# Performance work log

Hardware: AMD Instinct MI355X
Metric: run time of the kernel (lower is better)

## Reference

```python
import jax, jax.numpy as jnp
import numpy as np

B, S, D, H, DK, F, L, FEAT, T = 32, 256, 512, 8, 64, 2048, 6, 9, 100


def _pos_emb(seq_len, d):
    # 'transformers from scratch' style sinusoidal embedding
    pos = jnp.arange(seq_len, dtype=jnp.float32)[:, None]
    dim = jnp.arange(d, dtype=jnp.float32)[None, :]
    phase = pos / jnp.power(1e4, dim / d)
    return jnp.where(jnp.arange(d)[None, :] % 2 == 0, jnp.sin(phase), jnp.cos(phase))


def _ln(x, g, b, eps=1e-5):
    m = jnp.mean(x, -1, keepdims=True)
    v = jnp.mean((x - m) ** 2, -1, keepdims=True)
    return (x - m) * jax.lax.rsqrt(v + eps) * g + b


def _mha(q_in, k_in, v_in, wq, bq, wk, bk, wv, bv, wo, bo):
    # wq/wk/wv: [H, D, DK]; batched equivalent of per-head Linear projections
    q = jnp.einsum('bsd,hdk->bhsk', q_in, wq) + bq[:, None, :]
    k = jnp.einsum('bsd,hdk->bhsk', k_in, wk) + bk[:, None, :]
    v = jnp.einsum('bsd,hdk->bhsk', v_in, wv) + bv[:, None, :]
    scale = jnp.sqrt(jnp.asarray(q.shape[-1], jnp.float32))
    att = jax.nn.softmax(jnp.einsum('bhqk,bhsk->bhqs', q, k) / scale, axis=-1)
    o = jnp.einsum('bhqs,bhsv->bhqv', att, v)  # [B,H,S,DK]
    o = o.transpose(0, 2, 1, 3).reshape(q_in.shape[0], q_in.shape[1], -1)  # concat heads
    return o @ wo + bo


def setup_inputs() -> dict:
    key = jax.random.key(0)
    ks = iter(jax.random.split(key, 64))
    rn = lambda *sh: 0.02 * jax.random.normal(next(ks), sh, jnp.float32)
    d = {
        'tgt': jax.random.uniform(next(ks), (B, S, FEAT), jnp.float32),
        'memory': jax.random.normal(next(ks), (B, S, D), jnp.float32),
        'time': jax.random.randint(next(ks), (B, S), 0, T),
        'gender': jax.random.randint(next(ks), (B, 1), 0, 2),
        'race': jax.random.randint(next(ks), (B, 1), 0, 3),
        'mask': jax.random.uniform(next(ks), (B, S, FEAT), jnp.float32),
        'w_f2h': rn(FEAT, D), 'b_f2h': jnp.zeros((D,)),
        'emb_time': rn(T, D), 'emb_gender': rn(2, D), 'emb_race': rn(3, D),
        'wq1': rn(L, H, D, DK), 'bq1': jnp.zeros((L, H, DK)),
        'wk1': rn(L, H, D, DK), 'bk1': jnp.zeros((L, H, DK)),
        'wv1': rn(L, H, D, DK), 'bv1': jnp.zeros((L, H, DK)),
        'wo1': rn(L, H * DK, D), 'bo1': jnp.zeros((L, D)),
        'g1': jnp.ones((L, D)), 'be1': jnp.zeros((L, D)),
        'wq2': rn(L, H, D, DK), 'bq2': jnp.zeros((L, H, DK)),
        'wk2': rn(L, H, D, DK), 'bk2': jnp.zeros((L, H, DK)),
        'wv2': rn(L, H, D, DK), 'bv2': jnp.zeros((L, H, DK)),
        'wo2': rn(L, H * DK, D), 'bo2': jnp.zeros((L, D)),
        'g2': jnp.ones((L, D)), 'be2': jnp.zeros((L, D)),
        'w1f': rn(L, D, F), 'b1f': jnp.zeros((L, F)),
        'w2f': rn(L, F, D), 'b2f': jnp.zeros((L, D)),
        'gf': jnp.ones((L, D)), 'bff': jnp.zeros((L, D)),
        'w_out': rn(D, FEAT), 'b_out': jnp.zeros((FEAT,)),
        'w_m': rn(D, FEAT), 'b_m': jnp.zeros((FEAT,)),
    }
    return d


def reference(tgt, memory, time, gender, race, mask,
              w_f2h, b_f2h, emb_time, emb_gender, emb_race,
              wq1, bq1, wk1, bk1, wv1, bv1, wo1, bo1, g1, be1,
              wq2, bq2, wk2, bk2, wv2, bv2, wo2, bo2, g2, be2,
              w1f, b1f, w2f, b2f, gf, bff,
              w_out, b_out, w_m, b_m):
    # attentioned_mask=False, mask provided -> tgt = tgt * mask
    x = (tgt * mask) @ w_f2h + b_f2h  # feature2hidden
    x = x + _pos_emb(x.shape[1], x.shape[2])
    x = x + emb_time[time] + emb_gender[gender] + emb_race[race]  # [B,S,D] += [B,1,D]
    for l in range(L):
        # self-attention residual block (dropout is identity in eval)
        x = _ln(x + _mha(x, x, x, wq1[l], bq1[l], wk1[l], bk1[l], wv1[l], bv1[l], wo1[l], bo1[l]), g1[l], be1[l])
        # 'cross' block: q,k from memory, v from tgt; residual on tgt (tensors[-1])
        x = _ln(x + _mha(memory, memory, x, wq2[l], bq2[l], wk2[l], bk2[l], wv2[l], bv2[l], wo2[l], bo2[l]), g2[l], be2[l])
        # feed forward
        x = _ln(x + jax.nn.relu(x @ w1f[l] + b1f[l]) @ w2f[l] + b2f[l], gf[l], bff[l])
    output = jax.nn.sigmoid(x @ w_out + b_out)
    mask_out = jax.nn.sigmoid(x @ w_m + b_m)  # attentioned_mask=False -> linear_m(tgt)
    return output, time, mask_out
```

## Files before the change

### kernel.cpp

```cpp
#include <hip/hip_runtime.h>
#include <hip/hip_bf16.h>
#include <math.h>

constexpr int Bn   = 32;
constexpr int Sn   = 256;
constexpr int Dn   = 512;
constexpr int Hn   = 8;
constexpr int DKn  = 64;
constexpr int Fn   = 2048;
constexpr int Ln   = 6;
constexpr int FEATn= 9;
constexpr int BSn  = Bn * Sn;

typedef __hip_bfloat16 bf16;
typedef __attribute__((ext_vector_type(8))) short short8;
typedef __attribute__((ext_vector_type(4))) short short4v;
typedef __attribute__((ext_vector_type(4))) float f32x4;

#define GLOAD_LDS16(gp, lp)                                                   \
    __builtin_amdgcn_global_load_lds(                                         \
        (const __attribute__((address_space(1))) void*)(gp),                  \
        (__attribute__((address_space(3))) void*)(lp), 16, 0, 0)

#define BARRIER do {                                                          \
    __builtin_amdgcn_sched_barrier(0);                                        \
    asm volatile("" ::: "memory");                                            \
    __builtin_amdgcn_s_barrier();                                             \
    asm volatile("" ::: "memory");                                            \
    __builtin_amdgcn_sched_barrier(0);                                        \
} while (0)

#define VMCNT0 do {                                                           \
    asm volatile("s_waitcnt vmcnt(0)" ::: "memory");                          \
    __builtin_amdgcn_sched_barrier(0);                                        \
} while (0)

#define LGKM0 do {                                                            \
    asm volatile("s_waitcnt lgkmcnt(0)" ::: "memory");                        \
    __builtin_amdgcn_sched_barrier(0);                                        \
} while (0)

__device__ __forceinline__ short f2bs(float f) {
    __hip_bfloat16 h = __float2bfloat16(f);
    return *reinterpret_cast<short*>(&h);
}
__device__ __forceinline__ float bs2f(short s) {
    unsigned u = ((unsigned)(unsigned short)s) << 16;
    return *reinterpret_cast<float*>(&u);
}

__global__ __launch_bounds__(256)
void k_embed(const float* __restrict__ tgt, const float* __restrict__ mask,
             const float* __restrict__ w_f2h, const float* __restrict__ b_f2h,
             const int* __restrict__ timei, const int* __restrict__ gender,
             const int* __restrict__ race,
             const float* __restrict__ emb_t, const float* __restrict__ emb_g,
             const float* __restrict__ emb_r, bf16* __restrict__ x)
{
    int idx = blockIdx.x * 256 + threadIdx.x;
    int d  = idx & (Dn - 1);
    int bs = idx >> 9;
    int b  = bs / Sn;
    int s  = bs & (Sn - 1);
    const float* tg = tgt  + (size_t)bs * FEATn;
    const float* mk = mask + (size_t)bs * FEATn;
    float acc = b_f2h[d];
    #pragma unroll
    for (int f = 0; f < FEATn; ++f) acc += tg[f] * mk[f] * w_f2h[f * Dn + d];
    float phase = (float)s * expf(-((float)d / (float)Dn) * 9.210340372f);
    acc += (d & 1) ? cosf(phase) : sinf(phase);
    acc += emb_t[(size_t)timei[bs] * Dn + d];
    acc += emb_g[(size_t)gender[b] * Dn + d];
    acc += emb_r[(size_t)race[b]   * Dn + d];
    x[idx] = __float2bfloat16(acc);
}

__global__ __launch_bounds__(256)
void k_cvt(const float* __restrict__ in, bf16* __restrict__ out)
{
    int i = blockIdx.x * 256 + threadIdx.x;
    out[i] = __float2bfloat16(in[i]);
}

__global__ __launch_bounds__(256)
void k_tcvt6(const float* __restrict__ i0, bf16* __restrict__ o0,
             const float* __restrict__ i1, bf16* __restrict__ o1,
             const float* __restrict__ i2, bf16* __restrict__ o2,
             const float* __restrict__ i3, bf16* __restrict__ o3,
             const float* __restrict__ i4, bf16* __restrict__ o4,
             const float* __restrict__ i5, bf16* __restrict__ o5,
             int R, int C, int ZB)
{
    __shared__ float ts[32][33];
    const int sel = blockIdx.z / ZB, zi = blockIdx.z % ZB;
    const float* in  = sel == 0 ? i0 : sel == 1 ? i1 : sel == 2 ? i2
                     : sel == 3 ? i3 : sel == 4 ? i4 : i5;
    bf16*        out = sel == 0 ? o0 : sel == 1 ? o1 : sel == 2 ? o2
                     : sel == 3 ? o3 : sel == 4 ? o4 : o5;
    const int t  = threadIdx.x;
    const int tx = t & 31, ty = t >> 5;
    const int r0 = blockIdx.y * 32, c0 = blockIdx.x * 32;
    const size_t zo = (size_t)zi * R * C;
    #pragma unroll
    for (int i = 0; i < 4; ++i)
        ts[ty + 8 * i][tx] = in[zo + (size_t)(r0 + ty + 8 * i) * C + c0 + tx];
    __syncthreads();
    #pragma unroll
    for (int i = 0; i < 4; ++i)
        out[zo + (size_t)(c0 + ty + 8 * i) * R + r0 + tx] =
            __float2bfloat16(ts[tx][ty + 8 * i]);
}

__global__ __launch_bounds__(256)
void k_prep_final(const float* __restrict__ w_out, const float* __restrict__ b_out,
                  const float* __restrict__ w_m, const float* __restrict__ b_m,
                  bf16* __restrict__ Wcat, float* __restrict__ bcat)
{
    int idx = blockIdx.x * 256 + threadIdx.x;
    int n = idx >> 9, k = idx & 511;
    float v = 0.f;
    if (n < FEATn)          v = w_out[(size_t)k * FEATn + n];
    else if (n < 2 * FEATn) v = w_m[(size_t)k * FEATn + (n - FEATn)];
    Wcat[idx] = __float2bfloat16(v);
    if (idx < 32) {
        float bv = idx < FEATn ? b_out[idx]
                 : (idx < 2 * FEATn ? b_m[idx - FEATn] : 0.f);
        bcat[idx] = bv;
    }
}

template<int BN, bool RELU, bool RESID>
__global__ __launch_bounds__(256)
void k_gemm2ph(const bf16* __restrict__ Ain, const bf16* __restrict__ Win,
               const float* __restrict__ bia, const bf16* __restrict__ Rr,
               bf16* __restrict__ Cout, int M, int N, int K, int MTt, int NTt)
{
    constexpr int NT   = BN / 32;
    constexpr int NCB  = BN / 32;
    constexpr int BSZ  = BN * 64;
    constexpr int CSTR = BN + 8;
    constexpr int CPR  = BN / 8;
    __shared__ __align__(16) short smem[8192 + 2 * BSZ];

    const int id = blockIdx.x;
    const int cx = id & 7, j = id >> 3;
    const int mt = cx * (MTt >> 3) + j / NTt;
    const int nt = j % NTt;
    const int m0 = mt * 64, n0 = nt * BN;

    const int t = threadIdx.x, w = t >> 6, lane = t & 63;
    const int l16 = lane & 15, quad = lane >> 4;
    const int wm = (w & 1) * 32, wn = (w >> 1) * (BN / 2);

    const short* A = (const short*)Ain;
    const short* W = (const short*)Win;

    const int rowL = t >> 3;
    const int cX   = (t & 7) ^ (rowL & 7);
    const short* pA0 = A + (size_t)(m0 +  0 + rowL) * K + cX * 8;
    const short* pA1 = A + (size_t)(m0 + 32 + rowL) * K + cX * 8;
    const short* pB[NCB];
    #pragma unroll
    for (int i = 0; i < NCB; ++i)
        pB[i] = W + (size_t)(n0 + i * 32 + rowL) * K + cX * 8;

    auto stage = [&](int nb, int k2) {
        short* dA = smem + nb * 4096 + t * 8;
        short* dB = smem + 8192 + nb * BSZ + t * 8;
        GLOAD_LDS16(pA0 + (size_t)k2 * 64, dA);
        GLOAD_LDS16(pA1 + (size_t)k2 * 64, dA + 2048);
        #pragma unroll
        for (int i = 0; i < NCB; ++i)
            GLOAD_LDS16(pB[i] + (size_t)k2 * 64, dB + i * 2048);
    };

    const int axor  = (quad ^ (l16 & 7)) << 3;
    const int aBase = (wm + l16) * 64 + axor;
    const int bBase = 8192 + (wn + l16) * 64 + axor;

    float bias_v[NT];
    #pragma unroll
    for (int ni = 0; ni < NT; ++ni)
        bias_v[ni] = bia[n0 + wn + ni * 16 + l16];

    f32x4 acc[2][NT] = {};

    stage(0, 0);
    VMCNT0;
    BARRIER;

    const int NKT = K >> 6;
    for (int kt = 0; kt < NKT; ++kt) {
        const int bufA = (kt & 1) * 4096;
        const int bufB = (kt & 1) * BSZ;
        short8 af[2][2], bw[2][NT];
        #pragma unroll
        for (int mi = 0; mi < 2; ++mi) {
            const int a0 = bufA + aBase + mi * 1024;
            af[0][mi] = *(const short8*)(smem + a0);
            af[1][mi] = *(const short8*)(smem + (a0 ^ 32));
        }
        #pragma unroll
        for (int ni = 0; ni < NT; ++ni) {
            const int b0 = bufB + bBase + ni * 1024;
            bw[0][ni] = *(const short8*)(smem + b0);
            bw[1][ni] = *(const short8*)(smem + (b0 ^ 32));
        }
        if (kt + 1 < NKT) stage((kt + 1) & 1, kt + 1);
        LGKM0;
        __builtin_amdgcn_s_setprio(1);
        #pragma unroll
        for (int ks = 0; ks < 2; ++ks)
            #pragma unroll
            for (int mi = 0; mi < 2; ++mi)
                #pragma unroll
                for (int ni = 0; ni < NT; ++ni)
                    acc[mi][ni] = __builtin_amdgcn_mfma_f32_16x16x32_bf16(
                        af[ks][mi], bw[ks][ni], acc[mi][ni], 0, 0, 0);
        __builtin_amdgcn_s_setprio(0);
        VMCNT0;
        BARRIER;
    }

    #pragma unroll
    for (int mi = 0; mi < 2; ++mi)
        #pragma unroll
        for (int ni = 0; ni < NT; ++ni)
            #pragma unroll
            for (int r = 0; r < 4; ++r) {
                float v = acc[mi][ni][r] + bias_v[ni];
                if (RELU) v = fmaxf(v, 0.f);
                smem[(wm + mi * 16 + quad * 4 + r) * CSTR
                     + wn + ni * 16 + l16] = f2bs(v);
            }
    LGKM0;
    BARRIER;
    #pragma unroll
    for (int cc = 0; cc < 64 * CPR; cc += 256) {
        const int idx = cc + t;
        const int row = idx / CPR, colc = idx % CPR;
        const size_t goff = (size_t)(m0 + row) * N + n0 + colc * 8;
        short8 cv = *(const short8*)(smem + row * CSTR + colc * 8);
        if (RESID) {
            short8 rv = *(const short8*)((const short*)Rr + goff);
            short8 ov;
            #pragma unroll
            for (int i = 0; i < 8; ++i)
                ov[i] = f2bs(bs2f(cv[i]) + bs2f(rv[i]));
            *(short8*)((short*)Cout + goff) = ov;
        } else {
            *(short8*)((short*)Cout + goff) = cv;
        }
    }
}

template<int RH, int CH, class STG, class FIN>
__device__ __forceinline__ void gemm8_phase(short* sm, int buf, int baseA,
                                            int baseB, f32x4 (&acc)[8][4],
                                            STG stg, FIN fin)
{
    short8 paf[2][4];
    short8 pbf[2][2];
    #pragma unroll
    for (int i = 0; i < 4; ++i) {
        const int a0 = buf + baseA + RH * 4096 + i * 1024;
        paf[0][i] = *(const short8*)(sm + a0);
        paf[1][i] = *(const short8*)(sm + (a0 ^ 32));
    }
    #pragma unroll
    for (int j = 0; j < 2; ++j) {
        const int b0 = buf + baseB + CH * 2048 + j * 1024;
        pbf[0][j] = *(const short8*)(sm + b0);
        pbf[1][j] = *(const short8*)(sm + (b0 ^ 32));
    }
    stg();
    BARRIER;
    __builtin_amdgcn_s_setprio(1);
    #pragma unroll
    for (int i = 0; i < 4; ++i)
        #pragma unroll
        for (int j = 0; j < 2; ++j) {
            acc[RH * 4 + i][CH * 2 + j] = __builtin_amdgcn_mfma_f32_16x16x32_bf16(
                paf[0][i], pbf[0][j], acc[RH * 4 + i][CH * 2 + j], 0, 0, 0);
            acc[RH * 4 + i][CH * 2 + j] = __builtin_amdgcn_mfma_f32_16x16x32_bf16(
                paf[1][i], pbf[1][j], acc[RH * 4 + i][CH * 2 + j], 0, 0, 0);
        }
    __builtin_amdgcn_s_setprio(0);
    fin();
    BARRIER;
}

template<bool RELU>
__global__ __launch_bounds__(512, 2)
void k_gemm8ph(const bf16* __restrict__ Ain, const bf16* __restrict__ Win,
               const float* __restrict__ bia, bf16* __restrict__ Cout,
               int M, int N, int K, int NTt)
{
    __shared__ __align__(16) short smem[65536];

    const int id  = blockIdx.x;
    const int cxd = id & 7, jj = id >> 3;
    const int mpx = (M >> 8) >> 3;
    const int ml  = jj / NTt, nl = jj % NTt;
    const int mt  = cxd * mpx + ml;
    const int m0  = mt * 256, n0 = nl * 256;

    const int t    = threadIdx.x;
    const int lane = t & 63, w = t >> 6;
    const int l16  = lane & 15, quad = lane >> 4;
    const int wr   = w >> 2, wc = w & 3;

    const short* A = (const short*)Ain;
    const short* W = (const short*)Win;

    const int rowL = t >> 3;
    const int cX   = (t & 7) ^ (rowL & 7);
    const short* pA00 = A + (size_t)(m0 +   0 +  0 + rowL) * K + cX * 8;
    const short* pA01 = A + (size_t)(m0 +   0 + 64 + rowL) * K + cX * 8;
    const short* pA10 = A + (size_t)(m0 + 128 +  0 + rowL) * K + cX * 8;
    const short* pA11 = A + (size_t)(m0 + 128 + 64 + rowL) * K + cX * 8;
    const short* pB00 = W + (size_t)(n0 +   0 +  0 + rowL) * K + cX * 8;
    const short* pB01 = W + (size_t)(n0 +   0 + 64 + rowL) * K + cX * 8;
    const short* pB10 = W + (size_t)(n0 + 128 +  0 + rowL) * K + cX * 8;
    const short* pB11 = W + (size_t)(n0 + 128 + 64 + rowL) * K + cX * 8;

    auto stageA = [&](int nb, int k2) {
        short* d = smem + nb * 16384 + t * 8;
        GLOAD_LDS16(pA00 + (size_t)k2 * 64, d);
        GLOAD_LDS16(pA01 + (size_t)k2 * 64, d + 4096);
        GLOAD_LDS16(pA10 + (size_t)k2 * 64, d + 8192);
        GLOAD_LDS16(pA11 + (size_t)k2 * 64, d + 12288);
    };
    auto stageB = [&](int nb, int k2) {
        short* d = smem + 32768 + nb * 16384 + t * 8;
        GLOAD_LDS16(pB00 + (size_t)k2 * 64, d);
        GLOAD_LDS16(pB01 + (size_t)k2 * 64, d + 4096);
        GLOAD_LDS16(pB10 + (size_t)k2 * 64, d + 8192);
        GLOAD_LDS16(pB11 + (size_t)k2 * 64, d + 12288);
    };

    const int axor  = (quad ^ (l16 & 7)) << 3;
    const int baseA = wr * 8192 + l16 * 64 + axor;
    const int baseB = 32768 + (wc >> 1) * 8192 + (wc & 1) * 4096
                    + l16 * 64 + axor;

    float bias_v[4];
    #pragma unroll
    for (int ni = 0; ni < 4; ++ni)
        bias_v[ni] = bia[n0 + wc * 64 + ni * 16 + l16];

    f32x4 acc[8][4] = {};

    stageA(0, 0);
    stageB(0, 0);
    VMCNT0;
    BARRIER;

    const int NKT = K >> 6;
    for (int kt = 0; kt < NKT; ++kt) {
        const int  buf = (kt & 1) << 14;
        const int  nb  = (kt + 1) & 1;
        const bool st  = (kt + 1) < NKT;
        gemm8_phase<0, 0>(smem, buf, baseA, baseB, acc,
                          [&] { if (st) stageA(nb, kt + 1); }, [&] {});
        gemm8_phase<0, 1>(smem, buf, baseA, baseB, acc,
                          [&] { if (st) stageB(nb, kt + 1); }, [&] {});
        gemm8_phase<1, 0>(smem, buf, baseA, baseB, acc, [&] {}, [&] {});
        gemm8_phase<1, 1>(smem, buf, baseA, baseB, acc, [&] {}, [&] { VMCNT0; });
    }

    #pragma unroll
    for (int p = 0; p < 2; ++p) {
        if (wr == p) {
            #pragma unroll
            for (int mi = 0; mi < 8; ++mi)
                #pragma unroll
                for (int ni = 0; ni < 4; ++ni)
                    #pragma unroll
                    for (int r = 0; r < 4; ++r) {
                        float v = acc[mi][ni][r] + bias_v[ni];
                        if (RELU) v = fmaxf(v, 0.f);
                        smem[(mi * 16 + quad * 4 + r) * 264
                             + wc * 64 + ni * 16 + l16] = f2bs(v);
                    }
        }
        LGKM0;
        BARRIER;
        #pragma unroll
        for (int i2 = 0; i2 < 8; ++i2) {
            const int idx = i2 * 512 + t;
            const int row = idx >> 5, chn = idx & 31;
            short8 cv = *(const short8*)(smem + row * 264 + chn * 8);
            *(short8*)((short*)Cout + (size_t)(m0 + p * 128 + row) * N
                                     + n0 + chn * 8) = cv;
        }
        LGKM0;
        BARRIER;
    }
}

__global__ __launch_bounds__(512, 2)
void k_qkv8ph(const bf16* __restrict__ Aqk, const bf16* __restrict__ Av,
              const bf16* __restrict__ Wq, const bf16* __restrict__ Wk,
              const bf16* __restrict__ Wv,
              const float* __restrict__ bq, const float* __restrict__ bk,
              const float* __restrict__ bv,
              bf16* __restrict__ Cq, bf16* __restrict__ Ck,
              bf16* __restrict__ Vt)
{
    __shared__ __align__(16) short smem[65536];

    constexpr int K = Dn;
    const int id  = blockIdx.x;
    const int cxd = id & 7, jj = id >> 3;
    const int ml  = jj / 6, nl = jj % 6;
    const int mt  = cxd * 4 + ml;
    const int m0  = mt * 256;
    const int sel = nl >> 1;
    const int n0l = (nl & 1) * 256;

    const short* A = (const short*)(sel < 2 ? Aqk : Av);
    const short* W = (const short*)(sel == 0 ? Wq : sel == 1 ? Wk : Wv);
    const float* bia = sel == 0 ? bq : sel == 1 ? bk : bv;

    const int t    = threadIdx.x;
    const int lane = t & 63, w = t >> 6;
    const int l16  = lane & 15, quad = lane >> 4;
    const int wr   = w >> 2, wc = w & 3;

    const int rowL = t >> 3;
    const int cX   = (t & 7) ^ (rowL & 7);
    const short* pA00 = A + (size_t)(m0 +   0 +  0 + rowL) * K + cX * 8;
    const short* pA01 = A + (size_t)(m0 +   0 + 64 + rowL) * K + cX * 8;
    const short* pA10 = A + (size_t)(m0 + 128 +  0 + rowL) * K + cX * 8;
    const short* pA11 = A + (size_t)(m0 + 128 + 64 + rowL) * K + cX * 8;
    const short* pB00 = W + (size_t)(n0l +   0 +  0 + rowL) * K + cX * 8;
    const short* pB01 = W + (size_t)(n0l +   0 + 64 + rowL) * K + cX * 8;
    const short* pB10 = W + (size_t)(n0l + 128 +  0 + rowL) * K + cX * 8;
    const short* pB11 = W + (size_t)(n0l + 128 + 64 + rowL) * K + cX * 8;

    auto stageA = [&](int nb, int k2) {
        short* d = smem + nb * 16384 + t * 8;
        GLOAD_LDS16(pA00 + (size_t)k2 * 64, d);
        GLOAD_LDS16(pA01 + (size_t)k2 * 64, d + 4096);
        GLOAD_LDS16(pA10 + (size_t)k2 * 64, d + 8192);
        GLOAD_LDS16(pA11 + (size_t)k2 * 64, d + 12288);
    };
    auto stageB = [&](int nb, int k2) {
        short* d = smem + 32768 + nb * 16384 + t * 8;
        GLOAD_LDS16(pB00 + (size_t)k2 * 64, d);
        GLOAD_LDS16(pB01 + (size_t)k2 * 64, d + 4096);
        GLOAD_LDS16(pB10 + (size_t)k2 * 64, d + 8192);
        GLOAD_LDS16(pB11 + (size_t)k2 * 64, d + 12288);
    };

    const int axor  = (quad ^ (l16 & 7)) << 3;
    const int baseA = wr * 8192 + l16 * 64 + axor;
    const int baseB = 32768 + (wc >> 1) * 8192 + (wc & 1) * 4096
                    + l16 * 64 + axor;

    float bias_v[4];
    #pragma unroll
    for (int ni = 0; ni < 4; ++ni)
        bias_v[ni] = bia[n0l + wc * 64 + ni * 16 + l16];

    f32x4 acc[8][4] = {};

    stageA(0, 0);
    stageB(0, 0);
    VMCNT0;
    BARRIER;

    constexpr int NKT = K >> 6;
    for (int kt = 0; kt < NKT; ++kt) {
        const int  buf = (kt & 1) << 14;
        const int  nb  = (kt + 1) & 1;
        const bool st  = (kt + 1) < NKT;
        gemm8_phase<0, 0>(smem, buf, baseA, baseB, acc,
                          [&] { if (st) stageA(nb, kt + 1); }, [&] {});
        gemm8_phase<0, 1>(smem, buf, baseA, baseB, acc,
                          [&] { if (st) stageB(nb, kt + 1); }, [&] {});
        gemm8_phase<1, 0>(smem, buf, baseA, baseB, acc, [&] {}, [&] {});
        gemm8_phase<1, 1>(smem, buf, baseA, baseB, acc, [&] {}, [&] { VMCNT0; });
    }

    if (sel < 2) {
        bf16* C = sel == 0 ? Cq : Ck;
        #pragma unroll
        for (int p = 0; p < 2; ++p) {
            if (wr == p) {
                #pragma unroll
                for (int mi = 0; mi < 8; ++mi)
                    #pragma unroll
                    for (int ni = 0; ni < 4; ++ni)
                        #pragma unroll
                        for (int r = 0; r < 4; ++r)
                            smem[(mi * 16 + quad * 4 + r) * 264
                                 + wc * 64 + ni * 16 + l16] =
                                f2bs(acc[mi][ni][r] + bias_v[ni]);
            }
            LGKM0;
            BARRIER;
            #pragma unroll
            for (int i2 = 0; i2 < 8; ++i2) {
                const int idx = i2 * 512 + t;
                const int row = idx >> 5, chn = idx & 31;
                short8 cv = *(const short8*)(smem + row * 264 + chn * 8);
                *(short8*)((short*)C + (size_t)(m0 + p * 128 + row) * Dn
                                     + n0l + chn * 8) = cv;
            }
            LGKM0;
            BARRIER;
        }
    } else {
        #pragma unroll
        for (int p = 0; p < 4; ++p) {
            if (wc == p) {
                #pragma unroll
                for (int mi = 0; mi < 8; ++mi)
                    #pragma unroll
                    for (int ni = 0; ni < 4; ++ni)
                        #pragma unroll
                        for (int r = 0; r < 4; ++r)
                            smem[(ni * 16 + l16) * 264
                                 + wr * 128 + mi * 16 + quad * 4 + r] =
                                f2bs(acc[mi][ni][r] + bias_v[ni]);
            }
            LGKM0;
            BARRIER;
            #pragma unroll
            for (int i2 = 0; i2 < 4; ++i2) {
                const int idx = i2 * 512 + t;
                const int row = idx >> 5, chn = idx & 31;
                short8 cv = *(const short8*)(smem + row * 264 + chn * 8);
                *(short8*)((short*)Vt + (size_t)(n0l + p * 64 + row) * BSn
                                      + m0 + chn * 8) = cv;
            }
            LGKM0;
            BARRIER;
        }
    }
}

__global__ __launch_bounds__(256)
void k_attn_mfma(const bf16* __restrict__ q, const bf16* __restrict__ k,
                 const bf16* __restrict__ vT, bf16* __restrict__ ocat)
{
    __shared__ __align__(16) short smem[33280];
    short* Vst = smem;
    short* Ks  = smem + 16384;
    short* Ps  = smem + 16384;
    short* Cs  = smem + 16384;

    const int t = threadIdx.x, w = t >> 6, lane = t & 63;
    const int l16 = lane & 15, quad = lane >> 4;
    const int qt = blockIdx.x >> 8;
    const int bh = blockIdx.x & 255;
    const int h  = bh & 7;
    const int b  = bh >> 3;
    const int q0 = qt * 64;

    const short* kg = (const short*)k  + (size_t)b * Sn * Dn + h * DKn;
    const short* qg = (const short*)q  + (size_t)b * Sn * Dn + h * DKn;
    const short* vg = (const short*)vT + (size_t)h * DKn * BSn + b * Sn;

    #pragma unroll
    for (int i = 0; i < 8; ++i) {
        const int c   = w * 512 + i * 64 + lane;
        const int key = c >> 3, cgk = (c & 7) ^ (key & 7);
        GLOAD_LDS16(kg + (size_t)key * Dn + cgk * 8, Ks + (w * 512 + i * 64) * 8);
        const int dv = c >> 5, cgv = (c & 31) ^ (dv & 7);
        GLOAD_LDS16(vg + (size_t)dv * BSn + cgv * 8, Vst + (w * 512 + i * 64) * 8);
    }

    const short* qp = qg + (size_t)(q0 + w * 16 + l16) * Dn + quad * 8;
    short8 bq0 = *(const short8*)(qp);
    short8 bq1 = *(const short8*)(qp + 32);
    __syncthreads();

    f32x4 accs[16];
    #pragma unroll
    for (int mi = 0; mi < 16; ++mi) accs[mi] = f32x4{0.f, 0.f, 0.f, 0.f};
    #pragma unroll
    for (int mi = 0; mi < 16; ++mi) {
        const int key = mi * 16 + l16;
        const int r0s = (quad     ^ (key & 7)) * 8;
        const int r1s = ((quad+4) ^ (key & 7)) * 8;
        short8 af0 = *(const short8*)(Ks + key * 64 + r0s);
        short8 af1 = *(const short8*)(Ks + key * 64 + r1s);
        accs[mi] = __builtin_amdgcn_mfma_f32_16x16x32_bf16(af0, bq0, accs[mi], 0, 0, 0);
        accs[mi] = __builtin_amdgcn_mfma_f32_16x16x32_bf16(af1, bq1, accs[mi], 0, 0, 0);
    }

    float mx = -1e30f;
    #pragma unroll
    for (int mi = 0; mi < 16; ++mi)
        #pragma unroll
        for (int r = 0; r < 4; ++r) mx = fmaxf(mx, accs[mi][r]);
    mx = fmaxf(mx, __shfl_xor(mx, 16));
    mx = fmaxf(mx, __shfl_xor(mx, 32));
    float sum = 0.f;
    #pragma unroll
    for (int mi = 0; mi < 16; ++mi)
        #pragma unroll
        for (int r = 0; r < 4; ++r) {
            float e = __expf((accs[mi][r] - mx) * 0.125f);
            accs[mi][r] = e;
            sum += e;
        }
    sum += __shfl_xor(sum, 16);
    sum += __shfl_xor(sum, 32);
    const float rs = 1.f / sum;

    __syncthreads();

    short* pr = Ps + (w * 16 + l16) * 264;
    #pragma unroll
    for (int mi = 0; mi < 16; ++mi) {
        short4v pk;
        pk.x = f2bs(accs[mi][0] * rs);
        pk.y = f2bs(accs[mi][1] * rs);
        pk.z = f2bs(accs[mi][2] * rs);
        pk.w = f2bs(accs[mi][3] * rs);
        *(short4v*)(pr + mi * 16 + quad * 4) = pk;
    }
    __syncthreads();

    f32x4 acco[4];
    #pragma unroll
    for (int nt = 0; nt < 4; ++nt) acco[nt] = f32x4{0.f, 0.f, 0.f, 0.f};
    #pragma unroll
    for (int k0 = 0; k0 < 8; ++k0) {
        short8 pa = *(const short8*)(pr + k0 * 32 + quad * 8);
        #pragma unroll
        for (int nt = 0; nt < 4; ++nt) {
            const int dv = nt * 16 + l16;
            const int sl = ((4 * k0 + quad) ^ (dv & 7)) * 8;
            short8 vb = *(const short8*)(Vst + dv * 256 + sl);
            acco[nt] = __builtin_amdgcn_mfma_f32_16x16x32_bf16(pa, vb, acco[nt], 0, 0, 0);
        }
    }
    __syncthreads();

    #pragma unroll
    for (int nt = 0; nt < 4; ++nt)
        #pragma unroll
        for (int r = 0; r < 4; ++r)
            Cs[(w * 16 + quad * 4 + r) * 72 + nt * 16 + l16] = f2bs(acco[nt][r]);
    __syncthreads();
    #pragma unroll
    for (int c = 0; c < 512; c += 256) {
        const int row = (c + t) >> 3, colc = (c + t) & 7;
        short8 cv = *(const short8*)(Cs + row * 72 + colc * 8);
        *(short8*)((short*)ocat + (size_t)(b * Sn + q0 + row) * Dn
                                 + h * DKn + colc * 8) = cv;
    }
}

__global__ __launch_bounds__(256)
void k_ln(const bf16* __restrict__ y, const float* __restrict__ g,
          const float* __restrict__ be, bf16* __restrict__ xo)
{
    const int t = threadIdx.x, w = t >> 6, lane = t & 63;
    const int row = blockIdx.x * 4 + w;
    const short* yr = (const short*)y + (size_t)row * Dn + lane * 8;
    short8 v8 = *(const short8*)yr;
    float f[8];
    float s1 = 0.f, s2 = 0.f;
    #pragma unroll
    for (int i = 0; i < 8; ++i) {
        f[i] = bs2f(v8[i]);
        s1 += f[i];
        s2 += f[i] * f[i];
    }
    #pragma unroll
    for (int off = 1; off < 64; off <<= 1) {
        s1 += __shfl_xor(s1, off);
        s2 += __shfl_xor(s2, off);
    }
    const float mean = s1 * (1.f / Dn);
    const float var  = s2 * (1.f / Dn) - mean * mean;
    const float isd  = rsqrtf(var + 1e-5f);
    const float4 g0 = *(const float4*)(g  + lane * 8);
    const float4 g1 = *(const float4*)(g  + lane * 8 + 4);
    const float4 b0 = *(const float4*)(be + lane * 8);
    const float4 b1 = *(const float4*)(be + lane * 8 + 4);
    const float gg[8] = {g0.x, g0.y, g0.z, g0.w, g1.x, g1.y, g1.z, g1.w};
    const float bb[8] = {b0.x, b0.y, b0.z, b0.w, b1.x, b1.y, b1.z, b1.w};
    short8 o8;
    #pragma unroll
    for (int i = 0; i < 8; ++i)
        o8[i] = f2bs((f[i] - mean) * isd * gg[i] + bb[i]);
    *(short8*)((short*)xo + (size_t)row * Dn + lane * 8) = o8;
}

__global__ __launch_bounds__(256)
void k_final2(const bf16* __restrict__ x, const bf16* __restrict__ Wcat,
              const float* __restrict__ bcat, const int* __restrict__ timei,
              float* __restrict__ out)
{
    const int t = threadIdx.x, w = t >> 6, lane = t & 63;
    const int l16 = lane & 15, quad = lane >> 4;
    const int r0 = blockIdx.x * 64 + w * 16;
    const short* xp = (const short*)x + (size_t)(r0 + l16) * Dn + quad * 8;
    const short* wp = (const short*)Wcat + (size_t)l16 * Dn + quad * 8;

    f32x4 acc[2] = {};
    #pragma unroll
    for (int kk = 0; kk < 16; ++kk) {
        short8 af = *(const short8*)(xp + kk * 32);
        short8 b0 = *(const short8*)(wp + kk * 32);
        short8 b1 = *(const short8*)(wp + 16 * Dn + kk * 32);
        acc[0] = __builtin_amdgcn_mfma_f32_16x16x32_bf16(af, b0, acc[0], 0, 0, 0);
        acc[1] = __builtin_amdgcn_mfma_f32_16x16x32_bf16(af, b1, acc[1], 0, 0, 0);
    }

    #pragma unroll
    for (int nt = 0; nt < 2; ++nt) {
        const int col = nt * 16 + l16;
        const float bb = bcat[col];
        #pragma unroll
        for (int r = 0; r < 4; ++r) {
            const int row = r0 + quad * 4 + r;
            float v = acc[nt][r] + bb;
            float sg = 1.f / (1.f + expf(-v));
            if (col < FEATn)
                out[(size_t)row * FEATn + col] = sg;
            else if (col < 2 * FEATn)
                out[(size_t)BSn * FEATn + BSn + (size_t)row * FEATn + (col - FEATn)] = sg;
        }
    }
    if (l16 == 0) {
        #pragma unroll
        for (int r = 0; r < 4; ++r) {
            const int row = r0 + quad * 4 + r;
            out[(size_t)BSn * FEATn + row] = (float)timei[row];
        }
    }
}

extern "C" void kernel_launch(void* const* d_in, const int* in_sizes, int n_in,
                              void* d_out, int out_size, void* d_ws, size_t ws_size,
                              hipStream_t stream)
{
    const float* tgt    = (const float*)d_in[0];
    const float* memory = (const float*)d_in[1];
    const int*   timei  = (const int*)  d_in[2];
    const int*   gender = (const int*)  d_in[3];
    const int*   race   = (const int*)  d_in[4];
    const float* maskp  = (const float*)d_in[5];
    const float* w_f2h  = (const float*)d_in[6];
    const float* b_f2h  = (const float*)d_in[7];
    const float* emb_t  = (const float*)d_in[8];
    const float* emb_g  = (const float*)d_in[9];
    const float* emb_r  = (const float*)d_in[10];
    const float* wq1 = (const float*)d_in[11]; const float* bq1 = (const float*)d_in[12];
    const float* wk1 = (const float*)d_in[13]; const float* bk1 = (const float*)d_in[14];
    const float* wv1 = (const float*)d_in[15]; const float* bv1 = (const float*)d_in[16];
    const float* wo1 = (const float*)d_in[17]; const float* bo1 = (const float*)d_in[18];
    const float* g1  = (const float*)d_in[19]; const float* be1 = (const float*)d_in[20];
    const float* wq2 = (const float*)d_in[21]; const float* bq2 = (const float*)d_in[22];
    const float* wk2 = (const float*)d_in[23]; const float* bk2 = (const float*)d_in[24];
    const float* wv2 = (const float*)d_in[25]; const float* bv2 = (const float*)d_in[26];
    const float* wo2 = (const float*)d_in[27]; const float* bo2 = (const float*)d_in[28];
    const float* g2  = (const float*)d_in[29]; const float* be2 = (const float*)d_in[30];
    const float* w1f = (const float*)d_in[31]; const float* b1f = (const float*)d_in[32];
    const float* w2f = (const float*)d_in[33]; const float* b2f = (const float*)d_in[34];
    const float* gfp = (const float*)d_in[35]; const float* bff = (const float*)d_in[36];
    const float* w_out = (const float*)d_in[37]; const float* b_out = (const float*)d_in[38];
    const float* w_m   = (const float*)d_in[39]; const float* b_m   = (const float*)d_in[40];
    float* out = (float*)d_out;

    constexpr size_t WH  = 1572864;
    constexpr size_t WF  = 6291456;
    constexpr size_t NA  = (size_t)BSn * Dn;
    bf16* wsb   = (bf16*)d_ws;
    bf16* wq1t  = wsb;
    bf16* wk1t  = wq1t + WH;
    bf16* wv1t  = wk1t + WH;
    bf16* wo1t  = wv1t + WH;
    bf16* wq2t  = wo1t + WH;
    bf16* wk2t  = wq2t + WH;
    bf16* wv2t  = wk2t + WH;
    bf16* wo2t  = wv2t + WH;
    bf16* w1ft  = wo2t + WH;
    bf16* w2ft  = w1ft + WF;
    bf16* memb  = w2ft + WF;
    bf16* x     = memb + NA;
    bf16* b1    = x  + NA;
    bf16* b2    = b1 + NA;
    bf16* b3    = b2 + NA;
    bf16* b4    = b3 + NA;
    bf16* h1    = b1;
    bf16* wcat  = b4 + NA;
    float* bcat = (float*)(wcat + 32 * Dn);

    dim3 blk(256);

    k_tcvt6<<<dim3( 2, 16, 288), blk, 0, stream>>>(
        wq1, wq1t, wk1, wk1t, wv1, wv1t, wq2, wq2t, wk2, wk2t, wv2, wv2t,
        512, 64, 48);
    k_tcvt6<<<dim3(16, 16, 12), blk, 0, stream>>>(
        wo1, wo1t, wo2, wo2t, wo1, wo1t, wo1, wo1t, wo1, wo1t, wo1, wo1t,
        512, 512, 6);
    k_tcvt6<<<dim3(64, 16, 6), blk, 0, stream>>>(
        w1f, w1ft, w1f, w1ft, w1f, w1ft, w1f, w1ft, w1f, w1ft, w1f, w1ft,
        512, 2048, 6);
    k_tcvt6<<<dim3(16, 64, 6), blk, 0, stream>>>(
        w2f, w2ft, w2f, w2ft, w2f, w2ft, w2f, w2ft, w2f, w2ft, w2f, w2ft,
        2048, 512, 6);
    k_cvt <<<dim3(NA / 256), blk, 0, stream>>>(memory, memb);
    k_prep_final<<<dim3(64), blk, 0, stream>>>(w_out, b_out, w_m, b_m, wcat, bcat);

    k_embed<<<dim3((BSn * Dn) / 256), blk, 0, stream>>>(
        tgt, maskp, w_f2h, b_f2h, timei, gender, race, emb_t, emb_g, emb_r, x);

    dim3 gQ (192);
    dim3 gW (128 * 4);
    dim3 g8 (32 * 8);
    dim3 blk8(512);
    dim3 gA (Bn * Hn * 4);
    dim3 gL (BSn / 4);
    constexpr size_t WSL = 262144;
    constexpr size_t WFL = 1048576;

    for (int l = 0; l < Ln; ++l) {
        k_qkv8ph<<<gQ, blk8, 0, stream>>>(
            x, x,
            wq1t + l * WSL, wk1t + l * WSL, wv1t + l * WSL,
            bq1 + l * Dn, bk1 + l * Dn, bv1 + l * Dn,
            b1, b2, b3);
        k_attn_mfma<<<gA, blk, 0, stream>>>(b1, b2, b3, b4);
        k_gemm2ph<128, false, true><<<gW, blk, 0, stream>>>(
            b4, wo1t + l * WSL, bo1 + l * Dn, x, x, BSn, Dn, Dn, 128, 4);
        k_ln<<<gL, blk, 0, stream>>>(x, g1 + l * Dn, be1 + l * Dn, x);
        k_qkv8ph<<<gQ, blk8, 0, stream>>>(
            memb, x,
            wq2t + l * WSL, wk2t + l * WSL, wv2t + l * WSL,
            bq2 + l * Dn, bk2 + l * Dn, bv2 + l * Dn,
            b1, b2, b3);
        k_attn_mfma<<<gA, blk, 0, stream>>>(b1, b2, b3, b4);
        k_gemm2ph<128, false, true><<<gW, blk, 0, stream>>>(
            b4, wo2t + l * WSL, bo2 + l * Dn, x, x, BSn, Dn, Dn, 128, 4);
        k_ln<<<gL, blk, 0, stream>>>(x, g2 + l * Dn, be2 + l * Dn, x);
        k_gemm8ph<true><<<g8, blk8, 0, stream>>>(
            x, w1ft + l * WFL, b1f + l * Fn, h1, BSn, Fn, Dn, 8);
        k_gemm2ph<128, false, true><<<gW, blk, 0, stream>>>(
            h1, w2ft + l * WFL, b2f + l * Dn, x, x, BSn, Dn, Fn, 128, 4);
        k_ln<<<gL, blk, 0, stream>>>(x, gfp + l * Dn, bff + l * Dn, x);
    }

    k_final2<<<dim3(BSn / 64), blk, 0, stream>>>(x, wcat, bcat, timei, out);
}
```

Before: 1.313 ms.

## Process all 256 queries per block in attention, removing redundant K/V loads

Result: no change. 1.290 ms, median of 2 (-1.7%).

```diff
diff --git a/kernel.cpp b/kernel.cpp
--- a/kernel.cpp
+++ b/kernel.cpp
@@ -542,38 +542,35 @@
     }
 }
 
-__global__ __launch_bounds__(256)
+__global__ __launch_bounds__(1024)
 void k_attn_mfma(const bf16* __restrict__ q, const bf16* __restrict__ k,
                  const bf16* __restrict__ vT, bf16* __restrict__ ocat)
 {
-    __shared__ __align__(16) short smem[33280];
+    __shared__ __align__(16) short smem[65536];
     short* Vst = smem;
     short* Ks  = smem + 16384;
-    short* Ps  = smem + 16384;
-    short* Cs  = smem + 16384;
+    short* Ps  = smem + 32768;
 
     const int t = threadIdx.x, w = t >> 6, lane = t & 63;
     const int l16 = lane & 15, quad = lane >> 4;
-    const int qt = blockIdx.x >> 8;
-    const int bh = blockIdx.x & 255;
+    const int bh = blockIdx.x;
     const int h  = bh & 7;
     const int b  = bh >> 3;
-    const int q0 = qt * 64;
 
     const short* kg = (const short*)k  + (size_t)b * Sn * Dn + h * DKn;
     const short* qg = (const short*)q  + (size_t)b * Sn * Dn + h * DKn;
     const short* vg = (const short*)vT + (size_t)h * DKn * BSn + b * Sn;
 
     #pragma unroll
-    for (int i = 0; i < 8; ++i) {
-        const int c   = w * 512 + i * 64 + lane;
+    for (int i = 0; i < 2; ++i) {
+        const int c   = i * 1024 + w * 64 + lane;
         const int key = c >> 3, cgk = (c & 7) ^ (key & 7);
-        GLOAD_LDS16(kg + (size_t)key * Dn + cgk * 8, Ks + (w * 512 + i * 64) * 8);
+        GLOAD_LDS16(kg + (size_t)key * Dn + cgk * 8, Ks + (i * 1024 + w * 64) * 8);
         const int dv = c >> 5, cgv = (c & 31) ^ (dv & 7);
-        GLOAD_LDS16(vg + (size_t)dv * BSn + cgv * 8, Vst + (w * 512 + i * 64) * 8);
-    }
-
-    const short* qp = qg + (size_t)(q0 + w * 16 + l16) * Dn + quad * 8;
+        GLOAD_LDS16(vg + (size_t)dv * BSn + cgv * 8, Vst + (i * 1024 + w * 64) * 8);
+    }
+
+    const short* qp = qg + (size_t)(w * 16 + l16) * Dn + quad * 8;
     short8 bq0 = *(const short8*)(qp);
     short8 bq1 = *(const short8*)(qp + 32);
     __syncthreads();
@@ -612,47 +609,56 @@
     sum += __shfl_xor(sum, 32);
     const float rs = 1.f / sum;
 
-    __syncthreads();
-
-    short* pr = Ps + (w * 16 + l16) * 264;
-    #pragma unroll
-    for (int mi = 0; mi < 16; ++mi) {
-        short4v pk;
-        pk.x = f2bs(accs[mi][0] * rs);
-        pk.y = f2bs(accs[mi][1] * rs);
-        pk.z = f2bs(accs[mi][2] * rs);
-        pk.w = f2bs(accs[mi][3] * rs);
-        *(short4v*)(pr + mi * 16 + quad * 4) = pk;
-    }
-    __syncthreads();
+    short* pr = Ps + w * 2048 + l16 * 128;
+    const int psw = (l16 & 7) << 3;
 
     f32x4 acco[4];
     #pragma unroll
     for (int nt = 0; nt < 4; ++nt) acco[nt] = f32x4{0.f, 0.f, 0.f, 0.f};
-    #pragma unroll
-    for (int k0 = 0; k0 < 8; ++k0) {
-        short8 pa = *(const short8*)(pr + k0 * 32 + quad * 8);
-        #pragma unroll
-        for (int nt = 0; nt < 4; ++nt) {
-            const int dv = nt * 16 + l16;
-            const int sl = ((4 * k0 + quad) ^ (dv & 7)) * 8;
-            short8 vb = *(const short8*)(Vst + dv * 256 + sl);
-            acco[nt] = __builtin_amdgcn_mfma_f32_16x16x32_bf16(pa, vb, acco[nt], 0, 0, 0);
-        }
-    }
-    __syncthreads();
-
+
+    #pragma unroll
+    for (int half = 0; half < 2; ++half) {
+        if (half) LGKM0;
+        #pragma unroll
+        for (int mi = 0; mi < 8; ++mi) {
+            const int mg = half * 8 + mi;
+            short4v pk;
+            pk.x = f2bs(accs[mg][0] * rs);
+            pk.y = f2bs(accs[mg][1] * rs);
+            pk.z = f2bs(accs[mg][2] * rs);
+            pk.w = f2bs(accs[mg][3] * rs);
+            *(short4v*)(pr + ((mi * 16 + quad * 4) ^ psw)) = pk;
+        }
+        LGKM0;
+        #pragma unroll
+        for (int k0 = 0; k0 < 4; ++k0) {
+            short8 pa = *(const short8*)(pr + ((k0 * 32 + quad * 8) ^ psw));
+            #pragma unroll
+            for (int nt = 0; nt < 4; ++nt) {
+                const int dv = nt * 16 + l16;
+                const int ch = 4 * (half * 4 + k0) + quad;
+                const int sl = (ch ^ (dv & 7)) * 8;
+                short8 vb = *(const short8*)(Vst + dv * 256 + sl);
+                acco[nt] = __builtin_amdgcn_mfma_f32_16x16x32_bf16(
+                    pa, vb, acco[nt], 0, 0, 0);
+            }
+        }
+    }
+
+    LGKM0;
+    short* cs = Ps + w * 2048;
     #pragma unroll
     for (int nt = 0; nt < 4; ++nt)
         #pragma unroll
         for (int r = 0; r < 4; ++r)
-            Cs[(w * 16 + quad * 4 + r) * 72 + nt * 16 + l16] = f2bs(acco[nt][r]);
-    __syncthreads();
-    #pragma unroll
-    for (int c = 0; c < 512; c += 256) {
-        const int row = (c + t) >> 3, colc = (c + t) & 7;
-        short8 cv = *(const short8*)(Cs + row * 72 + colc * 8);
-        *(short8*)((short*)ocat + (size_t)(b * Sn + q0 + row) * Dn
+            cs[(quad * 4 + r) * 72 + nt * 16 + l16] = f2bs(acco[nt][r]);
+    LGKM0;
+    #pragma unroll
+    for (int j = 0; j < 2; ++j) {
+        const int idx = j * 64 + lane;
+        const int row = idx >> 3, colc = idx & 7;
+        short8 cv = *(const short8*)(cs + row * 72 + colc * 8);
+        *(short8*)((short*)ocat + (size_t)(b * Sn + w * 16 + row) * Dn
                                  + h * DKn + colc * 8) = cv;
     }
 }
@@ -819,7 +825,8 @@
     dim3 gW (128 * 4);
     dim3 g8 (32 * 8);
     dim3 blk8(512);
-    dim3 gA (Bn * Hn * 4);
+    dim3 gA (Bn * Hn);
+    dim3 blkA(1024);
     dim3 gL (BSn / 4);
     constexpr size_t WSL = 262144;
     constexpr size_t WFL = 1048576;
@@ -830,7 +837,7 @@
             wq1t + l * WSL, wk1t + l * WSL, wv1t + l * WSL,
             bq1 + l * Dn, bk1 + l * Dn, bv1 + l * Dn,
             b1, b2, b3);
-        k_attn_mfma<<<gA, blk, 0, stream>>>(b1, b2, b3, b4);
+        k_attn_mfma<<<gA, blkA, 0, stream>>>(b1, b2, b3, b4);
         k_gemm2ph<128, false, true><<<gW, blk, 0, stream>>>(
             b4, wo1t + l * WSL, bo1 + l * Dn, x, x, BSn, Dn, Dn, 128, 4);
         k_ln<<<gL, blk, 0, stream>>>(x, g1 + l * Dn, be1 + l * Dn, x);
@@ -839,7 +846,7 @@
             wq2t + l * WSL, wk2t + l * WSL, wv2t + l * WSL,
             bq2 + l * Dn, bk2 + l * Dn, bv2 + l * Dn,
             b1, b2, b3);
-        k_attn_mfma<<<gA, blk, 0, stream>>>(b1, b2, b3, b4);
+        k_attn_mfma<<<gA, blkA, 0, stream>>>(b1, b2, b3, b4);
         k_gemm2ph<128, false, true><<<gW, blk, 0, stream>>>(
             b4, wo2t + l * WSL, bo2 + l * Dn, x, x, BSn, Dn, Dn, 128, 4);
         k_ln<<<gL, blk, 0, stream>>>(x, g2 + l * Dn, be2 + l * Dn, x);
```
